# Kernel tuning notes

Hardware: AMD Instinct MI355X
Metric: run time of the kernel (lower is better)

The kernel has to match this reference:

```python
import jax, jax.numpy as jnp
import numpy as np

B, N, D, T = 256, 80, 1024, 3

def setup_inputs() -> dict:
    key = jax.random.key(0)
    ks = jax.random.split(key, 12)
    s = 0.02
    return {
        "x":   jax.random.normal(ks[0], (B, N, D), jnp.float32),
        "inM": jax.random.uniform(ks[1], (N, N), jnp.float32),
        "outM": jax.random.uniform(ks[2], (N, N), jnp.float32),
        "W1w": jax.random.normal(ks[3], (D, 2 * D), jnp.float32) * s,
        "b1w": jnp.zeros((D,), jnp.float32),
        "W1u": jax.random.normal(ks[4], (D, D), jnp.float32) * s,
        "b1u": jnp.zeros((D,), jnp.float32),
        "W2w": jax.random.normal(ks[5], (D, 2 * D), jnp.float32) * s,
        "b2w": jnp.zeros((D,), jnp.float32),
        "W2u": jax.random.normal(ks[6], (D, D), jnp.float32) * s,
        "b2u": jnp.zeros((D,), jnp.float32),
        "W3w": jax.random.normal(ks[7], (D, 2 * D), jnp.float32) * s,
        "b3w": jnp.zeros((D,), jnp.float32),
        "W3u": jax.random.normal(ks[8], (D, D), jnp.float32) * s,
        "b3u": jnp.zeros((D,), jnp.float32),
        "timeStep": T,
    }

def reference(x, inM, outM, W1w, b1w, W1u, b1u, W2w, b2w, W2u, b2u,
              W3w, b3w, W3u, b3u, timeStep):
    # x: [B, N, D]; inM/outM: [N, N] adjacency (same for every batch element)
    h = x
    for _ in range(timeStep):
        # propagation: aggregate along in- and out-edges, concat -> [B, N, 2D]
        a_in = jnp.einsum('nm,bmd->bnd', inM, h)
        a_out = jnp.einsum('nm,bmd->bnd', outM, h)
        a_c = jnp.concatenate([a_in, a_out], axis=-1)
        # GRU-style gated update (torch Linear: y = x @ W.T + b)
        z = jax.nn.sigmoid(a_c @ W1w.T + b1w + h @ W1u.T + b1u)
        r = jax.nn.sigmoid(a_c @ W2w.T + b2w + h @ W2u.T + b2u)
        h_c = jnp.tanh(a_c @ W3w.T + b3w + (r * h) @ W3u.T + b3u)
        h = (1.0 - z) * h + z * h_c
    return h
```

## Files before the change

### kernel.cpp

```cpp
#include <hip/hip_runtime.h>
#include <hip/hip_bf16.h>
#include <stdint.h>

#define B_   256
#define N_   80
#define D_   1024
#define M_   (B_*N_)
#define SA2_ 4096
#define SW_  6144
#define KT_  96

typedef _Float16 half_t;
typedef __attribute__((ext_vector_type(8))) _Float16 f16x8;
typedef __attribute__((ext_vector_type(4))) float f32x4;

__device__ __forceinline__ void async_cp16(const void* g, void* l) {
  __builtin_amdgcn_global_load_lds((const __attribute__((address_space(1))) unsigned int*)g,
                                   (__attribute__((address_space(3))) unsigned int*)l,
                                   16, 0, 0);
}
__device__ __forceinline__ float sigm_(float x) { return 1.0f / (1.0f + __expf(-x)); }
__device__ __forceinline__ float tanh_(float x) { return 2.0f / (1.0f + __expf(-2.0f * x)) - 1.0f; }
__device__ __forceinline__ void split_f16(float v, half_t& hi, half_t& lo) {
  hi = (half_t)v;
  lo = (half_t)(v - (float)hi);
}

__device__ __forceinline__ void plane_offsets(int kt, int UBASE, int& acol, int& whi, int& wlo) {
  if (kt < 64) { const int c = kt * 32;        acol = c;         whi = c;        wlo = 2048 + c; }
  else         { const int r = (kt - 64) * 32; acol = UBASE + r; whi = 4096 + r; wlo = 5120 + r; }
}

__global__ __launch_bounds__(256) void pack_weights(
    const float* __restrict__ W1w, const float* __restrict__ W1u,
    const float* __restrict__ W2w, const float* __restrict__ W2u,
    const float* __restrict__ W3w, const float* __restrict__ W3u,
    half_t* __restrict__ Wzr, half_t* __restrict__ Wh) {
  int idx = blockIdx.x * 256 + threadIdx.x;
  int n = idx / 3072, k = idx - n * 3072;
  const float *Ww, *Wu; int nr; half_t* outrow;
  if (n < 1024)      { Ww = W1w; Wu = W1u; nr = n;        outrow = Wzr + (size_t)n * SW_; }
  else if (n < 2048) { Ww = W2w; Wu = W2u; nr = n - 1024; outrow = Wzr + (size_t)n * SW_; }
  else               { Ww = W3w; Wu = W3u; nr = n - 2048; outrow = Wh + (size_t)(n - 2048) * SW_; }
  float v; int chi, clo;
  if (k < 2048) { v = Ww[nr * 2048 + k];          chi = k;               clo = 2048 + k; }
  else          { v = Wu[nr * 1024 + (k - 2048)]; chi = 4096 + (k-2048); clo = 5120 + (k - 2048); }
  half_t hi, lo; split_f16(v, hi, lo);
  outrow[chi] = hi; outrow[clo] = lo;
}

__global__ __launch_bounds__(256) void prop_kernel(
    const float* __restrict__ h, const float* __restrict__ inM,
    const float* __restrict__ outM, half_t* __restrict__ Abuf) {
  const int b = blockIdx.x;
  const int d = blockIdx.y * 256 + threadIdx.x;
  const float* hb = h + (size_t)b * N_ * D_ + d;
  float hreg[N_];
  #pragma unroll
  for (int m = 0; m < N_; ++m) hreg[m] = hb[m * D_];
  half_t* Ab = Abuf + (size_t)b * N_ * SA2_;
  #pragma unroll
  for (int m = 0; m < N_; ++m) Ab[m * SA2_ + 2048 + d] = (half_t)hreg[m];
  for (int n = 0; n < N_; ++n) {
    float ai = 0.f, ao = 0.f;
    #pragma unroll
    for (int m = 0; m < N_; ++m) {
      ai += inM[n * N_ + m] * hreg[m];
      ao += outM[n * N_ + m] * hreg[m];
    }
    Ab[n * SA2_ + d]        = (half_t)ai;
    Ab[n * SA2_ + 1024 + d] = (half_t)ao;
  }
}

template<bool IS_ZR>
__global__ __launch_bounds__(256, 3) void gemm_kernel(
    const half_t* __restrict__ Abuf,
    const half_t* __restrict__ W,
    const float* __restrict__ bw1, const float* __restrict__ bu1,
    const float* __restrict__ bw2, const float* __restrict__ bu2,
    const float* __restrict__ hcur,
    float* __restrict__ zbuf,
    half_t* __restrict__ rhbase,
    float* __restrict__ hout,
    int mtiles) {
  __shared__ f16x8 ldsA[640];
  __shared__ f16x8 ldsB[1024];

  const int ntiles = IS_ZR ? 16 : 8;
  int mt, nt;
  if ((mtiles & 7) == 0) {
    const int flat = blockIdx.x;
    const int strip = mtiles >> 3;
    const int xcd = flat & 7;
    const int loc = flat >> 3;
    mt = xcd * strip + loc / ntiles;
    nt = loc - (loc / ntiles) * ntiles;
  } else {
    mt = blockIdx.x / ntiles;
    nt = blockIdx.x - mt * ntiles;
  }
  const int m0 = mt * 160;
  const int n0 = nt * 128;

  const int tid  = threadIdx.x;
  const int lane = tid & 63;
  const int wave = tid >> 6;
  const int wm   = (wave & 1) * 80;
  const int wn   = (wave >> 1) * 64;
  const int l15  = lane & 15;
  const int l4   = lane >> 4;
  const int UBASE = IS_ZR ? 2048 : 3072;

  f32x4 acc[5][4];
  #pragma unroll
  for (int i = 0; i < 5; ++i)
    #pragma unroll
    for (int j = 0; j < 4; ++j) acc[i][j] = (f32x4){0.f, 0.f, 0.f, 0.f};

  const int arow = wm + l15;
  const int brow = wn + l15;
  const int aoff = arow * 4 + (l4 ^ ((arow >> 1) & 3));
  const int boff = brow * 4 + (l4 ^ ((brow >> 1) & 3));

  #define STAGE_TILE(ACOL, WHI, WLO) do {                                                      \
      _Pragma("unroll")                                                                        \
      for (int i_ = 0; i_ < 2; ++i_) {                                                         \
        const int cidx = i_ * 256 + tid;                                                       \
        const int q  = cidx & 3;                                                               \
        const int mm = cidx >> 2;                                                              \
        const int qg = q ^ ((mm >> 1) & 3);                                                    \
        async_cp16(Abuf + (size_t)(m0 + mm) * SA2_ + (ACOL) + qg * 8, &ldsA[cidx]);            \
      }                                                                                        \
      if (tid < 128) {                              \
        const int cidx = 512 + tid;                                                            \
        const int q  = cidx & 3;                                                               \
        const int mm = cidx >> 2;                                                              \
        const int qg = q ^ ((mm >> 1) & 3);                                                    \
        async_cp16(Abuf + (size_t)(m0 + mm) * SA2_ + (ACOL) + qg * 8, &ldsA[cidx]);            \
      }                                                                                        \
      _Pragma("unroll")                                                                        \
      for (int j_ = 0; j_ < 4; ++j_) {                                                         \
        const int cidx = j_ * 256 + tid;                                                       \
        const int pl = cidx >> 9;                                                              \
        const int q  = cidx & 3;                                                               \
        const int nn = (cidx >> 2) & 127;                                                      \
        const int qg = q ^ ((nn >> 1) & 3);                                                    \
        async_cp16(W + (size_t)(n0 + nn) * SW_ + (pl ? (WLO) : (WHI)) + qg * 8,                \
                   &ldsB[cidx]);                                                               \
      }                                                                                        \
    } while (0)

  int acol, whi, wlo;
  plane_offsets(0, UBASE, acol, whi, wlo);
  STAGE_TILE(acol, whi, wlo);

  for (int kt = 0; kt < KT_; ++kt) {
    asm volatile("s_waitcnt vmcnt(0)" ::: "memory");
    __syncthreads();

    f16x8 af[5], bb_h[4], bb_l[4];
    #pragma unroll
    for (int mi = 0; mi < 5; ++mi) af[mi] = ldsA[aoff + mi * 64];
    #pragma unroll
    for (int ni = 0; ni < 4; ++ni) { bb_h[ni] = ldsB[boff + ni * 64];
                                     bb_l[ni] = ldsB[512 + boff + ni * 64]; }
    __syncthreads();

    if (kt + 1 < KT_) {
      plane_offsets(kt + 1, UBASE, acol, whi, wlo);
      STAGE_TILE(acol, whi, wlo);
    }

    #pragma unroll
    for (int mi = 0; mi < 5; ++mi)
      #pragma unroll
      for (int ni = 0; ni < 4; ++ni)
        acc[mi][ni] = __builtin_amdgcn_mfma_f32_16x16x32_f16(af[mi], bb_h[ni], acc[mi][ni], 0, 0, 0);
    #pragma unroll
    for (int mi = 0; mi < 5; ++mi)
      #pragma unroll
      for (int ni = 0; ni < 4; ++ni)
        acc[mi][ni] = __builtin_amdgcn_mfma_f32_16x16x32_f16(af[mi], bb_l[ni], acc[mi][ni], 0, 0, 0);
  }
  #undef STAGE_TILE

  #pragma unroll
  for (int mi = 0; mi < 5; ++mi) {
    #pragma unroll
    for (int p = 0; p < 4; ++p) {
      const int m = m0 + wm + mi * 16 + l4 * 4 + p;
      #pragma unroll
      for (int ni = 0; ni < 4; ++ni) {
        const int n = n0 + wn + ni * 16 + l15;
        float v = acc[mi][ni][p];
        if (IS_ZR) {
          if (n < 1024) {
            zbuf[(size_t)m * 1024 + n] = sigm_(v + bw1[n] + bu1[n]);
          } else {
            const int nn2 = n - 1024;
            float r = sigm_(v + bw2[nn2] + bu2[nn2]);
            float rh = r * hcur[(size_t)m * 1024 + nn2];
            rhbase[(size_t)m * SA2_ + 3072 + nn2] = (half_t)rh;
          }
        } else {
          float hc = tanh_(v + bw1[n] + bu1[n]);
          float z  = zbuf[(size_t)m * 1024 + n];
          float ho = hcur[(size_t)m * 1024 + n];
          hout[(size_t)m * 1024 + n] = (1.0f - z) * ho + z * hc;
        }
      }
    }
  }
}

extern "C" void kernel_launch(void* const* d_in, const int* in_sizes, int n_in,
                              void* d_out, int out_size, void* d_ws, size_t ws_size,
                              hipStream_t stream) {
  const float* x    = (const float*)d_in[0];
  const float* inM  = (const float*)d_in[1];
  const float* outM = (const float*)d_in[2];
  const float* W1w  = (const float*)d_in[3];
  const float* b1w  = (const float*)d_in[4];
  const float* W1u  = (const float*)d_in[5];
  const float* b1u  = (const float*)d_in[6];
  const float* W2w  = (const float*)d_in[7];
  const float* b2w  = (const float*)d_in[8];
  const float* W2u  = (const float*)d_in[9];
  const float* b2u  = (const float*)d_in[10];
  const float* W3w  = (const float*)d_in[11];
  const float* b3w  = (const float*)d_in[12];
  const float* W3u  = (const float*)d_in[13];
  const float* b3u  = (const float*)d_in[14];
  float* hout = (float*)d_out;

  char* ws = (char*)d_ws;
  half_t* Wzr = (half_t*)ws;
  half_t* Wh  = (half_t*)(ws + 25165824);
  const size_t fixed = 37748736;
  int Rb = 256;
  while (Rb > 8 && fixed + (size_t)Rb * 983040ull > ws_size) Rb -= 8;
  float* zbuf = (float*)(ws + fixed);
  half_t* Abuf = (half_t*)(ws + fixed + (size_t)Rb * 327680ull);

  pack_weights<<<(3072 * 3072) / 256, 256, 0, stream>>>(
      W1w, W1u, W2w, W2u, W3w, W3u, Wzr, Wh);

  for (int t = 0; t < 3; ++t) {
    const float* hsrc = (t == 0) ? x : (const float*)hout;
    for (int b0 = 0; b0 < B_; b0 += Rb) {
      const int nb = (B_ - b0 < Rb) ? (B_ - b0) : Rb;
      const int rows = N_ * nb;
      const int mtiles = rows / 160;
      const float* hc = hsrc + (size_t)b0 * N_ * D_;
      prop_kernel<<<dim3(nb, D_ / 256), 256, 0, stream>>>(hc, inM, outM, Abuf);
      gemm_kernel<true><<<mtiles * 16, 256, 0, stream>>>(
          Abuf, Wzr, b1w, b1u, b2w, b2u, hc, zbuf, Abuf, nullptr, mtiles);
      gemm_kernel<false><<<mtiles * 8, 256, 0, stream>>>(
          Abuf, Wh, b3w, b3u, nullptr, nullptr, hc, zbuf, nullptr,
          hout + (size_t)b0 * N_ * D_, mtiles);
    }
  }
}
```

Before: 3.159 ms.

## Double-buffer LDS tiles with two-stage prefetch and partial vmcnt waits

Doubles the LDS A/B buffers and prefetches the k-tile two steps ahead, so that each iteration waits only for the older tile's loads through a partial vmcnt count instead of draining all outstanding global-to-LDS copies. The aim is to hide global load latency behind the MFMA work. LDS use doubles to about 48KB per block, which may limit the three blocks per CU requested by the launch bounds. The per-wave vmcnt values (7 vs 6) depend on how many copies each wave issues, which is fragile if the staging code changes.

```diff
diff --git a/kernel.cpp b/kernel.cpp
--- a/kernel.cpp
+++ b/kernel.cpp
@@ -13,6 +13,8 @@
 typedef _Float16 half_t;
 typedef __attribute__((ext_vector_type(8))) _Float16 f16x8;
 typedef __attribute__((ext_vector_type(4))) float f32x4;
+
+#define SB0() __builtin_amdgcn_sched_barrier(0)
 
 __device__ __forceinline__ void async_cp16(const void* g, void* l) {
   __builtin_amdgcn_global_load_lds((const __attribute__((address_space(1))) unsigned int*)g,
@@ -84,8 +86,8 @@
     half_t* __restrict__ rhbase,
     float* __restrict__ hout,
     int mtiles) {
-  __shared__ f16x8 ldsA[640];
-  __shared__ f16x8 ldsB[1024];
+  __shared__ f16x8 ldsA[1280];
+  __shared__ f16x8 ldsB[2048];
 
   const int ntiles = IS_ZR ? 16 : 8;
   int mt, nt;
@@ -123,21 +125,23 @@
   const int aoff = arow * 4 + (l4 ^ ((arow >> 1) & 3));
   const int boff = brow * 4 + (l4 ^ ((brow >> 1) & 3));
 
-  #define STAGE_TILE(ACOL, WHI, WLO) do {                                                      \
+  #define STAGE_TILE(BUF, ACOL, WHI, WLO) do {                                                 \
       _Pragma("unroll")                                                                        \
       for (int i_ = 0; i_ < 2; ++i_) {                                                         \
         const int cidx = i_ * 256 + tid;                                                       \
         const int q  = cidx & 3;                                                               \
         const int mm = cidx >> 2;                                                              \
         const int qg = q ^ ((mm >> 1) & 3);                                                    \
-        async_cp16(Abuf + (size_t)(m0 + mm) * SA2_ + (ACOL) + qg * 8, &ldsA[cidx]);            \
+        async_cp16(Abuf + (size_t)(m0 + mm) * SA2_ + (ACOL) + qg * 8,                          \
+                   &ldsA[(BUF) * 640 + cidx]);                                                 \
       }                                                                                        \
       if (tid < 128) {                              \
         const int cidx = 512 + tid;                                                            \
         const int q  = cidx & 3;                                                               \
         const int mm = cidx >> 2;                                                              \
         const int qg = q ^ ((mm >> 1) & 3);                                                    \
-        async_cp16(Abuf + (size_t)(m0 + mm) * SA2_ + (ACOL) + qg * 8, &ldsA[cidx]);            \
+        async_cp16(Abuf + (size_t)(m0 + mm) * SA2_ + (ACOL) + qg * 8,                          \
+                   &ldsA[(BUF) * 640 + cidx]);                                                 \
       }                                                                                        \
       _Pragma("unroll")                                                                        \
       for (int j_ = 0; j_ < 4; ++j_) {                                                         \
@@ -147,29 +151,45 @@
         const int nn = (cidx >> 2) & 127;                                                      \
         const int qg = q ^ ((nn >> 1) & 3);                                                    \
         async_cp16(W + (size_t)(n0 + nn) * SW_ + (pl ? (WLO) : (WHI)) + qg * 8,                \
-                   &ldsB[cidx]);                                                               \
+                   &ldsB[(BUF) * 1024 + cidx]);                                                \
       }                                                                                        \
     } while (0)
 
   int acol, whi, wlo;
   plane_offsets(0, UBASE, acol, whi, wlo);
-  STAGE_TILE(acol, whi, wlo);
+  STAGE_TILE(0, acol, whi, wlo);
+  plane_offsets(1, UBASE, acol, whi, wlo);
+  STAGE_TILE(1, acol, whi, wlo);
+
+  const bool wlohalf = (wave < 2);
 
   for (int kt = 0; kt < KT_; ++kt) {
-    asm volatile("s_waitcnt vmcnt(0)" ::: "memory");
-    __syncthreads();
-
+    if (kt < KT_ - 1) {
+      if (wlohalf) { asm volatile("s_waitcnt vmcnt(7)" ::: "memory"); }
+      else         { asm volatile("s_waitcnt vmcnt(6)" ::: "memory"); }
+    } else {
+      asm volatile("s_waitcnt vmcnt(0)" ::: "memory");
+    }
+    SB0();
+    __builtin_amdgcn_s_barrier();
+    SB0();
+
+    const int abase = (kt & 1) * 640;
+    const int bbase = (kt & 1) * 1024;
     f16x8 af[5], bb_h[4], bb_l[4];
     #pragma unroll
-    for (int mi = 0; mi < 5; ++mi) af[mi] = ldsA[aoff + mi * 64];
-    #pragma unroll
-    for (int ni = 0; ni < 4; ++ni) { bb_h[ni] = ldsB[boff + ni * 64];
-                                     bb_l[ni] = ldsB[512 + boff + ni * 64]; }
-    __syncthreads();
-
-    if (kt + 1 < KT_) {
-      plane_offsets(kt + 1, UBASE, acol, whi, wlo);
-      STAGE_TILE(acol, whi, wlo);
+    for (int mi = 0; mi < 5; ++mi) af[mi] = ldsA[abase + aoff + mi * 64];
+    #pragma unroll
+    for (int ni = 0; ni < 4; ++ni) { bb_h[ni] = ldsB[bbase + boff + ni * 64];
+                                     bb_l[ni] = ldsB[bbase + 512 + boff + ni * 64]; }
+    asm volatile("s_waitcnt lgkmcnt(0)" ::: "memory");
+    SB0();
+    __builtin_amdgcn_s_barrier();
+    SB0();
+
+    if (kt + 2 < KT_) {
+      plane_offsets(kt + 2, UBASE, acol, whi, wlo);
+      STAGE_TILE(kt & 1, acol, whi, wlo);
     }
 
     #pragma unroll
```

Measured after the change: 3.235 ms. +2.4%, slower.

## Double-buffer weight tiles in LDS and load activations directly to registers

Applied to the files above, without the earlier changes.

The A operand is no longer staged through LDS. Each lane now loads its activation fragments straight from global memory into registers, ping-ponging between two register sets. The weight tile is double-buffered in LDS, which removes the second barrier per K step so staging of the next tile overlaps the MFMAs, with sched_barrier placed around the barrier. This trades LDS traffic and one sync for more VGPR pressure and uncoalesced, per-lane global loads of A. The vmcnt(0) wait still blocks until the prefetch issued in the previous iteration completes.

```diff
diff --git a/kernel.cpp b/kernel.cpp
--- a/kernel.cpp
+++ b/kernel.cpp
@@ -13,6 +13,8 @@
 typedef _Float16 half_t;
 typedef __attribute__((ext_vector_type(8))) _Float16 f16x8;
 typedef __attribute__((ext_vector_type(4))) float f32x4;
+
+#define SB0() __builtin_amdgcn_sched_barrier(0)
 
 __device__ __forceinline__ void async_cp16(const void* g, void* l) {
   __builtin_amdgcn_global_load_lds((const __attribute__((address_space(1))) unsigned int*)g,
@@ -84,8 +86,7 @@
     half_t* __restrict__ rhbase,
     float* __restrict__ hout,
     int mtiles) {
-  __shared__ f16x8 ldsA[640];
-  __shared__ f16x8 ldsB[1024];
+  __shared__ f16x8 ldsB[2048];
 
   const int ntiles = IS_ZR ? 16 : 8;
   int mt, nt;
@@ -119,26 +120,11 @@
     for (int j = 0; j < 4; ++j) acc[i][j] = (f32x4){0.f, 0.f, 0.f, 0.f};
 
   const int arow = wm + l15;
+  const half_t* Arow0 = Abuf + (size_t)(m0 + arow) * SA2_ + l4 * 8;
   const int brow = wn + l15;
-  const int aoff = arow * 4 + (l4 ^ ((arow >> 1) & 3));
   const int boff = brow * 4 + (l4 ^ ((brow >> 1) & 3));
 
-  #define STAGE_TILE(ACOL, WHI, WLO) do {                                                      \
-      _Pragma("unroll")                                                                        \
-      for (int i_ = 0; i_ < 2; ++i_) {                                                         \
-        const int cidx = i_ * 256 + tid;                                                       \
-        const int q  = cidx & 3;                                                               \
-        const int mm = cidx >> 2;                                                              \
-        const int qg = q ^ ((mm >> 1) & 3);                                                    \
-        async_cp16(Abuf + (size_t)(m0 + mm) * SA2_ + (ACOL) + qg * 8, &ldsA[cidx]);            \
-      }                                                                                        \
-      if (tid < 128) {                              \
-        const int cidx = 512 + tid;                                                            \
-        const int q  = cidx & 3;                                                               \
-        const int mm = cidx >> 2;                                                              \
-        const int qg = q ^ ((mm >> 1) & 3);                                                    \
-        async_cp16(Abuf + (size_t)(m0 + mm) * SA2_ + (ACOL) + qg * 8, &ldsA[cidx]);            \
-      }                                                                                        \
+  #define STAGE_B(BUF, WHI, WLO) do {                                                          \
       _Pragma("unroll")                                                                        \
       for (int j_ = 0; j_ < 4; ++j_) {                                                         \
         const int cidx = j_ * 256 + tid;                                                       \
@@ -147,43 +133,56 @@
         const int nn = (cidx >> 2) & 127;                                                      \
         const int qg = q ^ ((nn >> 1) & 3);                                                    \
         async_cp16(W + (size_t)(n0 + nn) * SW_ + (pl ? (WLO) : (WHI)) + qg * 8,                \
-                   &ldsB[cidx]);                                                               \
+                   &ldsB[(BUF) * 1024 + cidx]);                                                \
       }                                                                                        \
     } while (0)
+  #define LOAD_A(DST, ACOL) do {                                                               \
+      _Pragma("unroll")                                                                        \
+      for (int mi_ = 0; mi_ < 5; ++mi_)                                                        \
+        DST[mi_] = *reinterpret_cast<const f16x8*>(Arow0 + (size_t)(mi_ * 16) * SA2_ + (ACOL));\
+    } while (0)
+
+  #define GEMM_ITER(KT, CUR, NXT) do {                                                         \
+      asm volatile("s_waitcnt vmcnt(0)" ::: "memory");    \
+      SB0();                                                                                   \
+      __builtin_amdgcn_s_barrier();                               \
+      SB0();                                                                                   \
+      if ((KT) + 1 < KT_) {                                                                    \
+        plane_offsets((KT) + 1, UBASE, acol, whi, wlo);                                        \
+        STAGE_B(((KT) + 1) & 1, whi, wlo);                                                     \
+        LOAD_A(NXT, acol);                                      \
+      }                                                                                        \
+      const int bbase = ((KT) & 1) * 1024;                                                     \
+      f16x8 bb[4];                                                                             \
+      _Pragma("unroll")                                                                        \
+      for (int ni = 0; ni < 4; ++ni) bb[ni] = ldsB[bbase + boff + ni * 64];                    \
+      _Pragma("unroll")                                                                        \
+      for (int mi = 0; mi < 5; ++mi)                                       \
+        _Pragma("unroll")                                                                      \
+        for (int ni = 0; ni < 4; ++ni)                                                         \
+          acc[mi][ni] = __builtin_amdgcn_mfma_f32_16x16x32_f16(CUR[mi], bb[ni], acc[mi][ni], 0, 0, 0); \
+      _Pragma("unroll")                                                                        \
+      for (int ni = 0; ni < 4; ++ni) bb[ni] = ldsB[bbase + 512 + boff + ni * 64];              \
+      _Pragma("unroll")                                                                        \
+      for (int mi = 0; mi < 5; ++mi)                                       \
+        _Pragma("unroll")                                                                      \
+        for (int ni = 0; ni < 4; ++ni)                                                         \
+          acc[mi][ni] = __builtin_amdgcn_mfma_f32_16x16x32_f16(CUR[mi], bb[ni], acc[mi][ni], 0, 0, 0); \
+    } while (0)
 
   int acol, whi, wlo;
   plane_offsets(0, UBASE, acol, whi, wlo);
-  STAGE_TILE(acol, whi, wlo);
-
-  for (int kt = 0; kt < KT_; ++kt) {
-    asm volatile("s_waitcnt vmcnt(0)" ::: "memory");
-    __syncthreads();
-
-    f16x8 af[5], bb_h[4], bb_l[4];
-    #pragma unroll
-    for (int mi = 0; mi < 5; ++mi) af[mi] = ldsA[aoff + mi * 64];
-    #pragma unroll
-    for (int ni = 0; ni < 4; ++ni) { bb_h[ni] = ldsB[boff + ni * 64];
-                                     bb_l[ni] = ldsB[512 + boff + ni * 64]; }
-    __syncthreads();
-
-    if (kt + 1 < KT_) {
-      plane_offsets(kt + 1, UBASE, acol, whi, wlo);
-      STAGE_TILE(acol, whi, wlo);
-    }
-
-    #pragma unroll
-    for (int mi = 0; mi < 5; ++mi)
-      #pragma unroll
-      for (int ni = 0; ni < 4; ++ni)
-        acc[mi][ni] = __builtin_amdgcn_mfma_f32_16x16x32_f16(af[mi], bb_h[ni], acc[mi][ni], 0, 0, 0);
-    #pragma unroll
-    for (int mi = 0; mi < 5; ++mi)
-      #pragma unroll
-      for (int ni = 0; ni < 4; ++ni)
-        acc[mi][ni] = __builtin_amdgcn_mfma_f32_16x16x32_f16(af[mi], bb_l[ni], acc[mi][ni], 0, 0, 0);
-  }
-  #undef STAGE_TILE
+  STAGE_B(0, whi, wlo);
+  f16x8 afA[5], afB[5];
+  LOAD_A(afA, acol);
+
+  for (int kt = 0; kt < KT_; kt += 2) {
+    GEMM_ITER(kt, afA, afB);
+    GEMM_ITER(kt + 1, afB, afA);
+  }
+  #undef GEMM_ITER
+  #undef STAGE_B
+  #undef LOAD_A
 
   #pragma unroll
   for (int mi = 0; mi < 5; ++mi) {
```

Measured after the change: 4.244 ms. +34.4%, slower.
